# Kernel tuning notes

Hardware: AMD Instinct MI355X
Metric: run time of the kernel (lower is better)

## Reference

```python
import jax, jax.numpy as jnp
import numpy as np

B, L, D, H = 8, 512, 1024, 16
HD = D // H  # head dim = 64
SCALE = 1.0  # scale=False in __init__


def _rel_sinusoid(seq_len, dim):
    # RelativeSinusoidalPositionalEmbedding lookup for relative positions
    # arange(-L/2, L/2) (even L), sinusoid of the raw relative position.
    half = dim // 2
    inv = jnp.exp(jnp.arange(half, dtype=jnp.float32) * (-(np.log(10000.0) / (half - 1))))
    r = jnp.arange(-(seq_len // 2), seq_len // 2, dtype=jnp.float32)  # (L,)
    ang = r[:, None] * inv[None, :]  # (L, half)
    return jnp.concatenate([jnp.sin(ang), jnp.cos(ang)], axis=1)  # (L, dim)


def setup_inputs() -> dict:
    key = jax.random.key(0)
    ks = jax.random.split(key, 8)
    s = 0.02
    x = jax.random.normal(ks[0], (B, L, D), jnp.float32)
    mask = jax.random.randint(ks[1], (B, L), 0, 2).astype(jnp.int64)
    mask = mask.at[:, 0].set(1)  # ensure at least one valid key per row
    qmask = jax.random.randint(ks[2], (B, L), 0, 2).astype(jnp.int64)
    w_qkv = jax.random.normal(ks[3], (D, 3 * D), jnp.float32) * s
    w_qkpos = jax.random.normal(ks[4], (HD, 2 * D), jnp.float32) * s
    w_fc = jax.random.normal(ks[5], (D, D), jnp.float32) * s
    b_fc = jnp.zeros((D,), jnp.float32)
    shift = jnp.abs(jax.random.normal(ks[6], (1,), jnp.float32)) + 0.001
    bias = -jnp.abs(jax.random.normal(ks[7], (1,), jnp.float32))
    return dict(x=x, mask=mask, qmask=qmask, w_qkv=w_qkv, w_qkpos=w_qkpos,
                w_fc=w_fc, b_fc=b_fc, shift=shift, bias=bias)


def reference(x, mask, qmask, w_qkv, w_qkpos, w_fc, b_fc, shift, bias):
    # trans_type='self', use_Gaussian=True, dropout in eval mode (identity)
    b, l, d = x.shape
    qkv = x @ w_qkv  # (B, L, 3D)
    q, k, v = jnp.split(qkv, 3, axis=-1)
    q = q.reshape(b, l, H, HD).transpose(0, 2, 1, 3)  # (B,H,L,hd)
    k = k.reshape(b, l, H, HD).transpose(0, 2, 1, 3)
    v = v.reshape(b, l, H, HD).transpose(0, 2, 1, 3)

    pe = _rel_sinusoid(l, HD)               # (L, hd)
    y = pe @ w_qkpos                        # (L, 2D)
    q_p, k_p = jnp.split(y, 2, axis=-1)     # (L, D) each
    q_p = q_p.reshape(l, H, HD).transpose(1, 0, 2)  # (H, L, hd)
    k_p = k_p.reshape(l, H, HD).transpose(1, 0, 2)  # (H, L, hd)

    attn = jnp.einsum('bhid,bhjd->bhij', q, k) + jnp.einsum('hid,hjd->hij', q_p, k_p)[None]

    # speaker-identity masking: zero out cross-speaker scores (trans_type='self')
    qsame = qmask[:, :, None] == qmask[:, None, :]  # (B, L, L)
    attn = jnp.where(qsame[:, None], attn, 0.0)
    attn = attn / SCALE

    # key padding mask -> -inf
    attn = jnp.where(mask[:, None, None, :] == 0, -jnp.inf, attn)

    # Gaussian distance bias: -(shift * (i-j)^2 + bias)
    idx = jnp.arange(l, dtype=jnp.float32)
    sqd = (idx[:, None] - idx[None, :]) ** 2  # (L, L)
    attn = attn + (-(shift[0] * sqd + bias[0]))[None, None]

    attn = jax.nn.softmax(attn, axis=-1)
    out = jnp.einsum('bhij,bhjd->bhid', attn, v)  # (B,H,L,hd)
    out = out.transpose(0, 2, 1, 3).reshape(b, l, d)
    return out @ w_fc + b_fc
```

## Files before the change

kernel.cpp:

```cpp
#include <hip/hip_runtime.h>
#include <hip/hip_bf16.h>

#define BB 8
#define LL 512
#define DD 1024
#define HH 16
#define HD 64
#define LOG2E 1.4426950408889634f

typedef __attribute__((ext_vector_type(8))) unsigned short u16x8;
typedef __attribute__((ext_vector_type(4))) unsigned short u16x4;
typedef __attribute__((ext_vector_type(8))) __bf16 bf16x8;
typedef __attribute__((ext_vector_type(4))) float f32x4;
typedef __attribute__((ext_vector_type(16))) float f32x16;

#define DEV __device__ __forceinline__

DEV unsigned short f2bf(float f) {
    return __builtin_bit_cast(unsigned short, (__bf16)f);
}
DEV f32x4 mfma16(u16x8 a, u16x8 b, f32x4 c) {
    return __builtin_amdgcn_mfma_f32_16x16x32_bf16(
        __builtin_bit_cast(bf16x8, a), __builtin_bit_cast(bf16x8, b), c, 0, 0, 0);
}
DEV f32x16 mfma32(u16x8 a, u16x8 b, f32x16 c) {
    return __builtin_amdgcn_mfma_f32_32x32x16_bf16(
        __builtin_bit_cast(bf16x8, a), __builtin_bit_cast(bf16x8, b), c, 0, 0, 0);
}
typedef __attribute__((address_space(1))) void gv_t;
typedef __attribute__((address_space(3))) void lv_t;
DEV void gload16(const void* g, void* l) {
    __builtin_amdgcn_global_load_lds((gv_t*)g, (lv_t*)l, 16, 0, 0);
}


__global__ __launch_bounds__(256) void cvt_x(const float* __restrict__ in,
                                             unsigned short* __restrict__ out) {
    int i = blockIdx.x * 256 + threadIdx.x;
    f32x4 v = *(const f32x4*)(in + i * 4);
    u16x4 o;
    o[0] = f2bf(v[0]); o[1] = f2bf(v[1]); o[2] = f2bf(v[2]); o[3] = f2bf(v[3]);
    *(u16x4*)(out + i * 4) = o;
}

__global__ __launch_bounds__(256) void transpose_cvt(
    const float* __restrict__ in, unsigned short* __restrict__ out,
    int R, int C) {
    __shared__ unsigned short tile[32][33];
    int c0 = blockIdx.x * 32, r0 = blockIdx.y * 32;
    int tx = threadIdx.x & 31, ty = threadIdx.x >> 5;
#pragma unroll
    for (int i = 0; i < 32; i += 8)
        tile[ty + i][tx] = f2bf(in[(r0 + ty + i) * C + c0 + tx]);
    __syncthreads();
#pragma unroll
    for (int i = 0; i < 32; i += 8)
        out[(c0 + ty + i) * R + r0 + tx] = tile[tx][ty + i];
}

__global__ __launch_bounds__(256) void posg(
    const float* __restrict__ w, unsigned short* __restrict__ qpx,
    unsigned short* __restrict__ kpx) {
    __shared__ float peS[64][64];
    __shared__ float wS[64][32];
    int c0 = blockIdx.x * 32, i0 = blockIdx.y * 64;
    int t = threadIdx.x;
#pragma unroll
    for (int j = 0; j < 16; ++j) {
        int o = t + j * 256;
        int ri = o >> 6, d = o & 63, dd = d & 31;
        float inv = expf((float)dd * -0.2971077539347156f);
        float ang = (float)(i0 + ri - 256) * inv;
        peS[ri][d] = (d < 32) ? sinf(ang) : cosf(ang);
    }
#pragma unroll
    for (int j = 0; j < 8; ++j) {
        int o = t + j * 256;
        wS[o >> 5][o & 31] = w[(o >> 5) * 2048 + c0 + (o & 31)];
    }
    __syncthreads();
#pragma unroll
    for (int j = 0; j < 8; ++j) {
        int o = t + j * 256;
        int row = o >> 5, col = o & 31;
        float acc = 0.0f;
#pragma unroll
        for (int k = 0; k < 64; ++k) acc += peS[row][k] * wS[k][col];
        int c = c0 + col, i = i0 + row;
        int qt = i >> 5, lq = i & 31;
        int cc = (c < 1024) ? c : (c - 1024);
        int h = cc >> 6, k = cc & 63;
        int ks = k >> 4, h2 = (k >> 3) & 1, jj = k & 7;
        unsigned idx = ((unsigned)(h * 4096 + qt * 256 + ks * 64 + h2 * 32 + lq)
                        << 3) + jj;
        if (c < 1024) qpx[idx] = f2bf(acc * LOG2E);
        else          kpx[idx] = f2bf(acc);
    }
}

template <int MODE>
__global__ __launch_bounds__(256) void gemm_bt(
    const unsigned short* __restrict__ A, const unsigned short* __restrict__ Bt,
    int M, int N, int K, int NBX, unsigned short* __restrict__ o0,
    unsigned short* __restrict__ o1, unsigned short* __restrict__ o2,
    float* __restrict__ fout, const float* __restrict__ bias) {
    __shared__ __align__(16) unsigned short As[128 * 32];
    __shared__ __align__(16) unsigned short Bs[128 * 32];
    int g = blockIdx.x;
    int swz = (g & 7) * (gridDim.x >> 3) + (g >> 3);
    int bx = swz % NBX, by = swz / NBX;
    int m0 = by * 128, n0 = bx * 128;
    int t = threadIdx.x;
    int w = t >> 6, l = t & 63, lg = l >> 4, lc = l & 15;
    int wr = w >> 1, wc = w & 1;

    f32x4 acc[4][4] = {};

    int sr = w * 16 + (l >> 2);
    int sk = (l & 3) * 8;
    const unsigned short* Ab = A + (m0 + sr) * K + sk;
    const unsigned short* Bb = Bt + (n0 + sr) * K + sk;
    unsigned short* dA0 = As + w * 512;
    unsigned short* dA1 = As + 2048 + w * 512;
    unsigned short* dB0 = Bs + w * 512;
    unsigned short* dB1 = Bs + 2048 + w * 512;

    for (int k0 = 0; k0 < K; k0 += 32) {
        __syncthreads();
        gload16(Ab + k0, dA0);
        gload16(Ab + 64 * K + k0, dA1);
        gload16(Bb + k0, dB0);
        gload16(Bb + 64 * K + k0, dB1);
        __syncthreads();
        u16x8 af[4], bf[4];
#pragma unroll
        for (int mm = 0; mm < 4; ++mm)
            af[mm] = *(const u16x8*)&As[(wr * 64 + mm * 16 + lc) * 32 + lg * 8];
#pragma unroll
        for (int nn = 0; nn < 4; ++nn)
            bf[nn] = *(const u16x8*)&Bs[(wc * 64 + nn * 16 + lc) * 32 + lg * 8];
#pragma unroll
        for (int mm = 0; mm < 4; ++mm)
#pragma unroll
            for (int nn = 0; nn < 4; ++nn)
                acc[mm][nn] = mfma16(af[mm], bf[nn], acc[mm][nn]);
    }

#pragma unroll
    for (int mm = 0; mm < 4; ++mm)
#pragma unroll
        for (int nn = 0; nn < 4; ++nn)
#pragma unroll
            for (int r = 0; r < 4; ++r) {
                int row = m0 + wr * 64 + mm * 16 + lg * 4 + r;
                int col = n0 + wc * 64 + nn * 16 + lc;
                float v = acc[mm][nn][r];
                if (MODE == 0) {
                    int bb = row >> 9, i = row & 511;
                    int which = col >> 10, dd = col & 1023;
                    int hh = dd >> 6, hd = dd & 63;
                    int bh2 = bb * HH + hh;
                    int tl = i >> 5, io = i & 31;
                    if (which == 2) {
                        int h2 = (io >> 2) & 1, ps = (io >> 4) & 1;
                        int j = (io & 3) | (((io >> 3) & 1) << 2);
                        int dblk = hd >> 5, lq = hd & 31;
                        unsigned idx = ((unsigned)(bh2 * 4096 + tl * 256 +
                                        (dblk * 2 + ps) * 64 + h2 * 32 + lq)
                                        << 3) + j;
                        o2[idx] = f2bf(v);
                    } else {
                        int ks = hd >> 4, h2 = (hd >> 3) & 1, j = hd & 7;
                        unsigned idx = ((unsigned)(bh2 * 4096 + tl * 256 +
                                        ks * 64 + h2 * 32 + io) << 3) + j;
                        if (which == 0) o0[idx] = f2bf(v * LOG2E);
                        else            o1[idx] = f2bf(v);
                    }
                } else {
                    fout[row * N + col] = v + bias[col];
                }
            }
}

__global__ __launch_bounds__(256, 4) void attn_k(
    const unsigned short* __restrict__ Qx, const unsigned short* __restrict__ Kx,
    const unsigned short* __restrict__ Vx, const unsigned short* __restrict__ QPx,
    const unsigned short* __restrict__ KPx, const int* __restrict__ mask,
    const int* __restrict__ qmask, const float* __restrict__ shp,
    unsigned short* __restrict__ out) {
    __shared__ float mbuf[2][64];
    __shared__ float lsbuf[2][64];
    __shared__ float obuf[2][64][33];

    int g = blockIdx.x;
    int bid = ((g & 7) << 7) + (g >> 3);
    int b = bid >> 7, h = (bid >> 3) & 15, qc = bid & 7;
    int t = threadIdx.x, w = t >> 6, l = t & 63;
    int qg = w & 1, kh = w >> 1;
    int lq = l & 31, hi = l >> 5;
    int q = qc * 64 + qg * 32 + lq;
    int bh = b * HH + h;
    int qt = qc * 2 + qg;

    const unsigned short* qb  = Qx  + (((unsigned)(bh * 4096 + qt * 256)) << 3) + (l << 3);
    const unsigned short* qpb = QPx + (((unsigned)(h  * 4096 + qt * 256)) << 3) + (l << 3);
    u16x8 qf[4], pf[4];
#pragma unroll
    for (int ks = 0; ks < 4; ++ks) {
        qf[ks] = *(const u16x8*)(qb + ks * 512);
        pf[ks] = *(const u16x8*)(qpb + ks * 512);
    }

    unsigned long long km[4], qm[4];
#pragma unroll
    for (int t8 = 0; t8 < 4; ++t8) {
        int base = b * LL + (kh * 4 + t8) * 64 + l;
        km[t8] = __ballot(mask[base] != 0);
        qm[t8] = __ballot(qmask[base] != 0);
    }
    int qi = (qmask[b * LL + q] != 0) ? 1 : 0;

    const float M0 = -1.0e30f, NEGF = -3.0e38f, THR = 8.0f;
    float negs = -(*shp) * LOG2E;
    float m = M0, ls = 0.0f;
    f32x16 o0 = {}, o1 = {};
    float fq = (float)(q - 4 * hi);

    for (int tt = 0; tt < 8; ++tt) {
        int ttg = kh * 8 + tt;
        const unsigned short* kb  = Kx  + (((unsigned)(bh * 4096 + ttg * 256)) << 3) + (l << 3);
        const unsigned short* kpb = KPx + (((unsigned)(h  * 4096 + ttg * 256)) << 3) + (l << 3);
        f32x16 sk = {}, sp = {};
#pragma unroll
        for (int ks = 0; ks < 4; ++ks) {
            sk = mfma32(*(const u16x8*)(kb + ks * 512), qf[ks], sk);
            sp = mfma32(*(const u16x8*)(kpb + ks * 512), pf[ks], sp);
        }

        unsigned kwn = ((unsigned)(km[tt >> 1] >> ((tt & 1) * 32))) >> (hi * 4);
        unsigned qwn = ((unsigned)(qm[tt >> 1] >> ((tt & 1) * 32))) >> (hi * 4);
        float bt = fq - 32.0f * (float)ttg;
        float p[16];
#pragma unroll
        for (int r = 0; r < 16; ++r) {
            const int off = (r & 3) + 8 * (r >> 2);
            float v = sk[r] + sp[r];
            v = (((qwn >> off) & 1u) == (unsigned)qi) ? v : 0.0f;
            float dr = bt - (float)off;
            v = __builtin_fmaf(negs * dr, dr, v);
            v = ((kwn >> off) & 1u) ? v : NEGF;
            p[r] = v;
        }
        float a0 = fmaxf(fmaxf(p[0], p[1]), fmaxf(p[2], p[3]));
        float a1 = fmaxf(fmaxf(p[4], p[5]), fmaxf(p[6], p[7]));
        float a2 = fmaxf(fmaxf(p[8], p[9]), fmaxf(p[10], p[11]));
        float a3 = fmaxf(fmaxf(p[12], p[13]), fmaxf(p[14], p[15]));
        float pmax = fmaxf(fmaxf(a0, a1), fmaxf(a2, a3));
        pmax = fmaxf(pmax, __shfl_xor(pmax, 32));
        if (!__all(pmax <= m + THR)) {
            float mn = fmaxf(m, pmax);
            float sc = __builtin_amdgcn_exp2f(m - mn);
#pragma unroll
            for (int r = 0; r < 16; ++r) { o0[r] *= sc; o1[r] *= sc; }
            ls *= sc;
            m = mn;
        }
#pragma unroll
        for (int r = 0; r < 16; ++r) p[r] = __builtin_amdgcn_exp2f(p[r] - m);
        ls += (((p[0] + p[1]) + (p[2] + p[3])) + ((p[4] + p[5]) + (p[6] + p[7]))) +
              (((p[8] + p[9]) + (p[10] + p[11])) +
               ((p[12] + p[13]) + (p[14] + p[15])));
        u16x8 pf0, pf1;
#pragma unroll
        for (int j = 0; j < 8; ++j) { pf0[j] = f2bf(p[j]); pf1[j] = f2bf(p[8 + j]); }
        const unsigned short* vb = Vx + (((unsigned)(bh * 4096 + ttg * 256)) << 3) + (l << 3);
        o0 = mfma32(*(const u16x8*)(vb), pf0, o0);
        o0 = mfma32(*(const u16x8*)(vb + 512), pf1, o0);
        o1 = mfma32(*(const u16x8*)(vb + 1024), pf0, o1);
        o1 = mfma32(*(const u16x8*)(vb + 1536), pf1, o1);
    }

    if (kh == 1) {
        mbuf[qg][l] = m;
        lsbuf[qg][l] = ls;
#pragma unroll
        for (int r = 0; r < 16; ++r) {
            obuf[qg][l][r] = o0[r];
            obuf[qg][l][16 + r] = o1[r];
        }
    }
    __syncthreads();
    if (kh == 0) {
        float m1 = mbuf[qg][l], ls1 = lsbuf[qg][l];
        float mm = fmaxf(m, m1);
        float sc0 = __builtin_amdgcn_exp2f(m - mm);
        float sc1 = __builtin_amdgcn_exp2f(m1 - mm);
        float lsm = ls * sc0 + ls1 * sc1;
        float rs = lsm + __shfl_xor(lsm, 32);
        float rinv = __builtin_amdgcn_rcpf(rs);
        unsigned short* ob = out + ((long)(b * LL + q)) * DD + h * HD + hi * 4;
#pragma unroll
        for (int rg = 0; rg < 4; ++rg) {
            u16x4 pk0, pk1;
#pragma unroll
            for (int rr = 0; rr < 4; ++rr) {
                int i = rg * 4 + rr;
                float v0 = __builtin_fmaf(o0[i], sc0, obuf[qg][l][i] * sc1);
                float v1 = __builtin_fmaf(o1[i], sc0, obuf[qg][l][16 + i] * sc1);
                pk0[rr] = f2bf(v0 * rinv);
                pk1[rr] = f2bf(v1 * rinv);
            }
            *(u16x4*)(ob + rg * 8) = pk0;
            *(u16x4*)(ob + 32 + rg * 8) = pk1;
        }
    }
}

extern "C" void kernel_launch(void* const* d_in, const int* in_sizes, int n_in,
                              void* d_out, int out_size, void* d_ws,
                              size_t ws_size, hipStream_t stream) {
    const float* x     = (const float*)d_in[0];
    const int*   mask  = (const int*)d_in[1];
    const int*   qmask = (const int*)d_in[2];
    const float* w_qkv = (const float*)d_in[3];
    const float* w_qkp = (const float*)d_in[4];
    const float* w_fc  = (const float*)d_in[5];
    const float* b_fc  = (const float*)d_in[6];
    const float* shift = (const float*)d_in[7];

    char* ws = (char*)d_ws;
    unsigned short* xb   = (unsigned short*)(ws);
    unsigned short* qb   = (unsigned short*)(ws + 8388608);
    unsigned short* kb   = (unsigned short*)(ws + 16777216);
    unsigned short* vtb  = (unsigned short*)(ws + 25165824);
    unsigned short* qp   = (unsigned short*)(ws + 33554432);
    unsigned short* kp   = (unsigned short*)(ws + 34603008);
    unsigned short* wqt  = (unsigned short*)(ws + 35651584);
    unsigned short* wft  = (unsigned short*)(ws + 41943040);
    unsigned short* aout = (unsigned short*)(ws + 44040192);

    cvt_x<<<4096, 256, 0, stream>>>(x, xb);
    transpose_cvt<<<dim3(96, 32), 256, 0, stream>>>(w_qkv, wqt, 1024, 3072);
    transpose_cvt<<<dim3(32, 32), 256, 0, stream>>>(w_fc, wft, 1024, 1024);
    posg<<<dim3(64, 8), 256, 0, stream>>>(w_qkp, qp, kp);
    gemm_bt<0><<<768, 256, 0, stream>>>(xb, wqt, 4096, 3072, 1024, 24, qb, kb,
                                        vtb, nullptr, nullptr);
    attn_k<<<1024, 256, 0, stream>>>(qb, kb, vtb, qp, kp, mask, qmask, shift,
                                     aout);
    gemm_bt<1><<<256, 256, 0, stream>>>(aout, wft, 4096, 1024, 1024, 8, nullptr,
                                        nullptr, nullptr, (float*)d_out, b_fc);
}
```

Before: 137.7 us.

## Fuse x bf16 conversion into QKV GEMM, swizzle LDS, hoist V loads in attention

The separate fp32-to-bf16 conversion kernel for x is removed. The QKV GEMM now loads fp32 x directly, converts it in registers, prefetches the next k-slice and writes to LDS. Both GEMM LDS tiles use an XOR swizzle on the 8-element column group to reduce bank conflicts. The attention kernel drops its launch-bounds occupancy hint, fully unrolls the key-tile loop and issues the V loads early so they overlap with the score computation. In exchange, register pressure rises and attention occupancy may drop, and the A-tile global reads become synchronous register loads instead of direct-to-LDS loads.

New measurement: 141.4 us. +2.7%, slower.

```diff
diff --git a/kernel.cpp b/kernel.cpp
--- a/kernel.cpp
+++ b/kernel.cpp
@@ -33,15 +33,6 @@
     __builtin_amdgcn_global_load_lds((gv_t*)g, (lv_t*)l, 16, 0, 0);
 }
 
-
-__global__ __launch_bounds__(256) void cvt_x(const float* __restrict__ in,
-                                             unsigned short* __restrict__ out) {
-    int i = blockIdx.x * 256 + threadIdx.x;
-    f32x4 v = *(const f32x4*)(in + i * 4);
-    u16x4 o;
-    o[0] = f2bf(v[0]); o[1] = f2bf(v[1]); o[2] = f2bf(v[2]); o[3] = f2bf(v[3]);
-    *(u16x4*)(out + i * 4) = o;
-}
 
 __global__ __launch_bounds__(256) void transpose_cvt(
     const float* __restrict__ in, unsigned short* __restrict__ out,
@@ -100,7 +91,8 @@
 
 template <int MODE>
 __global__ __launch_bounds__(256) void gemm_bt(
-    const unsigned short* __restrict__ A, const unsigned short* __restrict__ Bt,
+    const float* __restrict__ Af, const unsigned short* __restrict__ Abf,
+    const unsigned short* __restrict__ Bt,
     int M, int N, int K, int NBX, unsigned short* __restrict__ o0,
     unsigned short* __restrict__ o1, unsigned short* __restrict__ o2,
     float* __restrict__ fout, const float* __restrict__ bias) {
@@ -116,29 +108,65 @@
 
     f32x4 acc[4][4] = {};
 
-    int sr = w * 16 + (l >> 2);
-    int sk = (l & 3) * 8;
-    const unsigned short* Ab = A + (m0 + sr) * K + sk;
-    const unsigned short* Bb = Bt + (n0 + sr) * K + sk;
+    int sr = t >> 2;
+    int sc = (t & 3) ^ ((t >> 3) & 3);
+    const unsigned short* Bb = Bt + (n0 + sr) * K + sc * 8;
+    unsigned short* dB0 = Bs + w * 512;
+    unsigned short* dB1 = Bs + 2048 + w * 512;
+
+    const float* Axf = nullptr;
+    const unsigned short* Ab = nullptr;
     unsigned short* dA0 = As + w * 512;
     unsigned short* dA1 = As + 2048 + w * 512;
-    unsigned short* dB0 = Bs + w * 512;
-    unsigned short* dB1 = Bs + 2048 + w * 512;
+    f32x4 pa00, pa01, pa10, pa11;
+    if (MODE == 0) {
+        Axf = Af + (m0 + sr) * K + (t & 3) * 8;
+        pa00 = *(const f32x4*)(Axf);
+        pa01 = *(const f32x4*)(Axf + 4);
+        pa10 = *(const f32x4*)(Axf + 64 * K);
+        pa11 = *(const f32x4*)(Axf + 64 * K + 4);
+    } else {
+        Ab = Abf + (m0 + sr) * K + sc * 8;
+    }
+    int wA0 = sr * 32 + sc * 8;
+    int wA1 = (sr + 64) * 32 + sc * 8;
+    int rsw = (lc >> 1) & 3;
 
     for (int k0 = 0; k0 < K; k0 += 32) {
         __syncthreads();
-        gload16(Ab + k0, dA0);
-        gload16(Ab + 64 * K + k0, dA1);
-        gload16(Bb + k0, dB0);
-        gload16(Bb + 64 * K + k0, dB1);
+        if (MODE == 0) {
+            u16x8 wv0, wv1;
+#pragma unroll
+            for (int j = 0; j < 4; ++j) {
+                wv0[j] = f2bf(pa00[j]); wv0[4 + j] = f2bf(pa01[j]);
+                wv1[j] = f2bf(pa10[j]); wv1[4 + j] = f2bf(pa11[j]);
+            }
+            *(u16x8*)&As[wA0] = wv0;
+            *(u16x8*)&As[wA1] = wv1;
+            gload16(Bb + k0, dB0);
+            gload16(Bb + 64 * K + k0, dB1);
+            if (k0 + 32 < K) {
+                pa00 = *(const f32x4*)(Axf + k0 + 32);
+                pa01 = *(const f32x4*)(Axf + k0 + 36);
+                pa10 = *(const f32x4*)(Axf + 64 * K + k0 + 32);
+                pa11 = *(const f32x4*)(Axf + 64 * K + k0 + 36);
+            }
+        } else {
+            gload16(Ab + k0, dA0);
+            gload16(Ab + 64 * K + k0, dA1);
+            gload16(Bb + k0, dB0);
+            gload16(Bb + 64 * K + k0, dB1);
+        }
         __syncthreads();
         u16x8 af[4], bf[4];
 #pragma unroll
         for (int mm = 0; mm < 4; ++mm)
-            af[mm] = *(const u16x8*)&As[(wr * 64 + mm * 16 + lc) * 32 + lg * 8];
+            af[mm] = *(const u16x8*)&As[(wr * 64 + mm * 16 + lc) * 32 +
+                                        ((lg ^ rsw) << 3)];
 #pragma unroll
         for (int nn = 0; nn < 4; ++nn)
-            bf[nn] = *(const u16x8*)&Bs[(wc * 64 + nn * 16 + lc) * 32 + lg * 8];
+            bf[nn] = *(const u16x8*)&Bs[(wc * 64 + nn * 16 + lc) * 32 +
+                                        ((lg ^ rsw) << 3)];
 #pragma unroll
         for (int mm = 0; mm < 4; ++mm)
 #pragma unroll
@@ -182,7 +210,7 @@
             }
 }
 
-__global__ __launch_bounds__(256, 4) void attn_k(
+__global__ void attn_k(
     const unsigned short* __restrict__ Qx, const unsigned short* __restrict__ Kx,
     const unsigned short* __restrict__ Vx, const unsigned short* __restrict__ QPx,
     const unsigned short* __restrict__ KPx, const int* __restrict__ mask,
@@ -226,10 +254,16 @@
     f32x16 o0 = {}, o1 = {};
     float fq = (float)(q - 4 * hi);
 
+#pragma unroll
     for (int tt = 0; tt < 8; ++tt) {
         int ttg = kh * 8 + tt;
         const unsigned short* kb  = Kx  + (((unsigned)(bh * 4096 + ttg * 256)) << 3) + (l << 3);
         const unsigned short* kpb = KPx + (((unsigned)(h  * 4096 + ttg * 256)) << 3) + (l << 3);
+        const unsigned short* vb  = Vx  + (((unsigned)(bh * 4096 + ttg * 256)) << 3) + (l << 3);
+        u16x8 vf0 = *(const u16x8*)(vb);
+        u16x8 vf1 = *(const u16x8*)(vb + 512);
+        u16x8 vf2 = *(const u16x8*)(vb + 1024);
+        u16x8 vf3 = *(const u16x8*)(vb + 1536);
         f32x16 sk = {}, sp = {};
 #pragma unroll
         for (int ks = 0; ks < 4; ++ks) {
@@ -273,11 +307,10 @@
         u16x8 pf0, pf1;
 #pragma unroll
         for (int j = 0; j < 8; ++j) { pf0[j] = f2bf(p[j]); pf1[j] = f2bf(p[8 + j]); }
-        const unsigned short* vb = Vx + (((unsigned)(bh * 4096 + ttg * 256)) << 3) + (l << 3);
-        o0 = mfma32(*(const u16x8*)(vb), pf0, o0);
-        o0 = mfma32(*(const u16x8*)(vb + 512), pf1, o0);
-        o1 = mfma32(*(const u16x8*)(vb + 1024), pf0, o1);
-        o1 = mfma32(*(const u16x8*)(vb + 1536), pf1, o1);
+        o0 = mfma32(vf0, pf0, o0);
+        o0 = mfma32(vf1, pf1, o0);
+        o1 = mfma32(vf2, pf0, o1);
+        o1 = mfma32(vf3, pf1, o1);
     }
 
     if (kh == 1) {
@@ -329,7 +362,6 @@
     const float* shift = (const float*)d_in[7];
 
     char* ws = (char*)d_ws;
-    unsigned short* xb   = (unsigned short*)(ws);
     unsigned short* qb   = (unsigned short*)(ws + 8388608);
     unsigned short* kb   = (unsigned short*)(ws + 16777216);
     unsigned short* vtb  = (unsigned short*)(ws + 25165824);
@@ -339,14 +371,14 @@
     unsigned short* wft  = (unsigned short*)(ws + 41943040);
     unsigned short* aout = (unsigned short*)(ws + 44040192);
 
-    cvt_x<<<4096, 256, 0, stream>>>(x, xb);
     transpose_cvt<<<dim3(96, 32), 256, 0, stream>>>(w_qkv, wqt, 1024, 3072);
     transpose_cvt<<<dim3(32, 32), 256, 0, stream>>>(w_fc, wft, 1024, 1024);
     posg<<<dim3(64, 8), 256, 0, stream>>>(w_qkp, qp, kp);
-    gemm_bt<0><<<768, 256, 0, stream>>>(xb, wqt, 4096, 3072, 1024, 24, qb, kb,
-                                        vtb, nullptr, nullptr);
+    gemm_bt<0><<<768, 256, 0, stream>>>(x, nullptr, wqt, 4096, 3072, 1024, 24,
+                                        qb, kb, vtb, nullptr, nullptr);
     attn_k<<<1024, 256, 0, stream>>>(qb, kb, vtb, qp, kp, mask, qmask, shift,
                                      aout);
-    gemm_bt<1><<<256, 256, 0, stream>>>(aout, wft, 4096, 1024, 1024, 8, nullptr,
-                                        nullptr, nullptr, (float*)d_out, b_fc);
-}
+    gemm_bt<1><<<256, 256, 0, stream>>>(nullptr, aout, wft, 4096, 1024, 1024, 8,
+                                        nullptr, nullptr, nullptr,
+                                        (float*)d_out, b_fc);
+}
```
